# Optimization experiments

Hardware: AMD Instinct MI355X
Metric: run time of the kernel (lower is better)

The kernel has to match this reference:

```python
import jax, jax.numpy as jnp
import numpy as np

N_FFT = 512; HOP = 256; WIN = 512
FDRC = 0.5; ORDER = 5; SPKS = 2
NFREQ = N_FFT // 2 + 1           # 257
HID = 512
PROJ = 2 * ORDER * SPKS * NFREQ  # 5140
LN_EPS = 1e-5
_WINDOW = 0.5 - 0.5 * jnp.cos(2 * jnp.pi * jnp.arange(WIN) / WIN)  # periodic hann


def _stft(x):
    # x: [B, L] -> complex spec [B, F, T], center-padded (reflect), hann window
    pad = N_FFT // 2
    xp = jnp.pad(x, ((0, 0), (pad, pad)), mode='reflect')
    T = 1 + (xp.shape[1] - N_FFT) // HOP
    idx = jnp.arange(T)[:, None] * HOP + jnp.arange(N_FFT)[None, :]
    frames = xp[:, idx] * _WINDOW            # [B, T, n_fft]
    spec = jnp.fft.rfft(frames, axis=-1)     # [B, T, F]
    return spec.transpose(0, 2, 1)           # [B, F, T]


def _istft(spec, length):
    # spec: [B, F, T] complex -> waveform [B, length] via overlap-add with window-square norm
    pad = N_FFT // 2
    frames = jnp.fft.irfft(spec.transpose(0, 2, 1), n=N_FFT, axis=-1) * _WINDOW  # [B,T,n_fft]
    B, T, _ = frames.shape
    total = length + 2 * pad
    idx = (jnp.arange(T)[:, None] * HOP + jnp.arange(N_FFT)[None, :]).ravel()
    out = jnp.zeros((B, total), frames.dtype).at[:, idx].add(frames.reshape(B, -1))
    wsq = jnp.zeros((total,), frames.dtype).at[idx].add(jnp.tile(_WINDOW ** 2, T))
    seg = wsq[pad:pad + length]
    return out[:, pad:pad + length] / jnp.where(seg > 1e-11, seg, 1.0)


def _lstm(xs, W_ih, W_hh, b_ih, b_hh):
    # xs: [T, B, in]; torch gate order i,f,g,o; returns hidden sequence [T, B, H]
    T, B, _ = xs.shape
    H = W_hh.shape[1]
    xs_proj = xs @ W_ih.T + (b_ih + b_hh)    # hoist input projection out of scan

    def step(carry, xp_t):
        h, c = carry
        gates = xp_t + h @ W_hh.T
        i, f, g, o = jnp.split(gates, 4, axis=-1)
        c = jax.nn.sigmoid(f) * c + jax.nn.sigmoid(i) * jnp.tanh(g)
        h = jax.nn.sigmoid(o) * jnp.tanh(c)
        return (h, c), h

    init = (jnp.zeros((B, H), xs.dtype), jnp.zeros((B, H), xs.dtype))
    _, hs = jax.lax.scan(step, init, xs_proj)
    return hs


def setup_inputs() -> dict:
    key = jax.random.key(0)
    ks = jax.random.split(key, 14)
    s = 0.04  # ~ 1/sqrt(hidden)
    return {
        'x': jax.random.normal(ks[0], (32, 160000), dtype=jnp.float32),
        'ln_g': jnp.ones((NFREQ,), jnp.float32),
        'ln_b': jnp.zeros((NFREQ,), jnp.float32),
        'W_ih0': jax.random.normal(ks[1], (4 * HID, NFREQ), jnp.float32) * s,
        'W_hh0': jax.random.normal(ks[2], (4 * HID, HID), jnp.float32) * s,
        'b_ih0': jax.random.normal(ks[3], (4 * HID,), jnp.float32) * s,
        'b_hh0': jax.random.normal(ks[4], (4 * HID,), jnp.float32) * s,
        'W_ih1': jax.random.normal(ks[5], (4 * HID, HID), jnp.float32) * s,
        'W_hh1': jax.random.normal(ks[6], (4 * HID, HID), jnp.float32) * s,
        'b_ih1': jax.random.normal(ks[7], (4 * HID,), jnp.float32) * s,
        'b_hh1': jax.random.normal(ks[8], (4 * HID,), jnp.float32) * s,
        'proj_W': jax.random.normal(ks[9], (PROJ, HID), jnp.float32) * s,
        'proj_b': jax.random.normal(ks[10], (PROJ,), jnp.float32) * s,
    }


def reference(x, ln_g, ln_b, W_ih0, W_hh0, b_ih0, b_hh0,
              W_ih1, W_hh1, b_ih1, b_hh1, proj_W, proj_b):
    B, L = x.shape
    spec = _stft(x)                      # [B, F, T] complex
    T = spec.shape[-1]
    mag = jnp.abs(spec) ** FDRC          # [B, F, T]

    # full-band sequence model (pre-LN -> 2-layer LSTM -> proj -> tanh)
    h = mag.transpose(2, 0, 1)           # [T, B, F]
    mu = h.mean(-1, keepdims=True)
    var = h.var(-1, keepdims=True)
    h = (h - mu) / jnp.sqrt(var + LN_EPS) * ln_g + ln_b
    h = _lstm(h, W_ih0, W_hh0, b_ih0, b_hh0)
    h = _lstm(h, W_ih1, W_hh1, b_ih1, b_hh1)
    h = jnp.tanh(h @ proj_W.T + proj_b)  # [T, B, 2*d*s*F]
    fb = h.transpose(1, 2, 0)            # [B, 2*d*s*F, T]

    # deep-filter coefficients: 'b (c d s f) t -> b d s f t c' -> complex [B,d,s,F,T]
    coef = fb.reshape(B, 2, ORDER, SPKS, NFREQ, T)
    coef_c = jax.lax.complex(coef[:, 0], coef[:, 1])

    # unfold spectrogram along time with left pad of (order-1): [B, F, T, d]
    padded = jnp.pad(spec, ((0, 0), (0, 0), (ORDER - 1, 0)))
    spec_unf = jnp.stack([padded[:, :, d:d + T] for d in range(ORDER)], axis=-1)

    # out[b,s,f,t] = sum_d spec_unf[b,f,t,d] * coef[b,d,s,f,t]
    enh = jnp.einsum('bftd,bdsft->bsft', spec_unf, coef_c)  # [B, S, F, T]

    enh_y = _istft(enh.reshape(B * SPKS, NFREQ, T), L).reshape(B, SPKS, L)
    return enh_y
```

## Files before the change

### kernel.cpp

```cpp
#include <hip/hip_runtime.h>
#include <hip/hip_cooperative_groups.h>
#include <math.h>

#define BATCH 32
#define LEN   160000
#define NFFT  512
#define NT    626
#define NF    257
#define NFP   288
#define HID   512
#define PROJN 5140
#define TC    32
#define NCHUNK 20
#define K0    800
#define K1    1024
#define NLSTM 64
#define NWORK 192
#define NBLKT 256

typedef unsigned short ushort;
typedef __attribute__((ext_vector_type(8))) short short8;
typedef __attribute__((ext_vector_type(4))) float f32x4;

__device__ __forceinline__ float sigm(float x){ return 1.0f/(1.0f+expf(-x)); }
__device__ __forceinline__ ushort f2bf(float f){
  union{float f;unsigned u;} v; v.f=f;
  unsigned r = v.u + 0x7fffu + ((v.u>>16)&1u);
  return (ushort)(r>>16);
}

__global__ __launch_bounds__(256) void k_setup(float* tw, int* zr, int nz,
                                               float* h1slot0, int nh1s,
                                               float* outz, int nout,
                                               const float* __restrict__ Wih0, const float* __restrict__ Whh0,
                                               const float* __restrict__ bih0, const float* __restrict__ bhh0,
                                               const float* __restrict__ Wih1, const float* __restrict__ Whh1,
                                               const float* __restrict__ bih1, const float* __restrict__ bhh1,
                                               const float* __restrict__ projW,
                                               ushort* __restrict__ W0, ushort* __restrict__ W1,
                                               float* __restrict__ b0c, float* __restrict__ b1c,
                                               ushort* __restrict__ projWb){
  const int gsz = gridDim.x*256;
  int gid = blockIdx.x*256 + threadIdx.x;
  if (gid < 512){
    float ang = 6.28318530717958647692f * (float)gid / 512.0f;
    tw[gid]     = cosf(ang);
    tw[512+gid] = sinf(ang);
  }
  for (int j = gid; j < nz; j += gsz) zr[j] = 0;
  for (int j = gid; j < nh1s; j += gsz) h1slot0[j] = 0.f;
  for (int j = gid; j < nout; j += gsz) outz[j] = 0.f;
  const int n0 = 2048*K0, n1 = 2048*K1, n2 = PROJN*HID;
  for (int i = gid; i < n0 + n1 + 4096 + n2; i += gsz){
    if (i < n0){
      int r = i / K0, c = i - r*K0;
      float v = (c < 257) ? Wih0[(size_t)r*257 + c] : (c < NFP ? 0.f : Whh0[(size_t)r*512 + (c-NFP)]);
      W0[i] = f2bf(v);
    } else if (i < n0 + n1){
      int j = i - n0;
      int r = j / K1, c = j - r*K1;
      float v = (c < 512) ? Wih1[(size_t)r*512 + c] : Whh1[(size_t)r*512 + (c-512)];
      W1[j] = f2bf(v);
    } else if (i < n0 + n1 + 4096){
      int j = i - n0 - n1;
      if (j < 2048) b0c[j] = bih0[j] + bhh0[j];
      else          b1c[j-2048] = bih1[j-2048] + bhh1[j-2048];
    } else {
      int j = i - n0 - n1 - 4096;
      projWb[j] = f2bf(projW[j]);
    }
  }
}

__global__ __launch_bounds__(256) void k_stftln(const float* __restrict__ x, const float* __restrict__ tw,
                                                const float* __restrict__ g, const float* __restrict__ be,
                                                ushort* __restrict__ hlnb){
  int b = blockIdx.x / NT;
  int t = blockIdx.x % NT;
  __shared__ float fr[NFFT], mg[NF];
  __shared__ float red[16];
  const float* xb = x + (size_t)b*LEN;
  for (int n = threadIdx.x; n < NFFT; n += 256){
    int j = t*256 + n - 256;
    if (j < 0) j = -j;
    else if (j >= LEN) j = 2*LEN - 2 - j;
    fr[n] = xb[j] * (0.5f - 0.5f*tw[n]);
  }
  __syncthreads();
  float v=0.f, v2=0.f;
  for (int f = threadIdx.x; f < NF; f += 256){
    float c4 = tw[(4*f)&511], s4 = tw[512+((4*f)&511)];
    float cr0=1.f,            si0=0.f;
    float cr1=tw[f&511],      si1=tw[512+(f&511)];
    float cr2=tw[(2*f)&511],  si2=tw[512+((2*f)&511)];
    float cr3=tw[(3*f)&511],  si3=tw[512+((3*f)&511)];
    float ar0=0.f,ai0=0.f,ar1=0.f,ai1=0.f,ar2=0.f,ai2=0.f,ar3=0.f,ai3=0.f;
    #pragma unroll 4
    for (int n = 0; n < NFFT; n += 4){
      ar0 += fr[n  ]*cr0; ai0 -= fr[n  ]*si0;
      ar1 += fr[n+1]*cr1; ai1 -= fr[n+1]*si1;
      ar2 += fr[n+2]*cr2; ai2 -= fr[n+2]*si2;
      ar3 += fr[n+3]*cr3; ai3 -= fr[n+3]*si3;
      float tc, ts;
      tc = cr0*c4 - si0*s4; ts = cr0*s4 + si0*c4; cr0=tc; si0=ts;
      tc = cr1*c4 - si1*s4; ts = cr1*s4 + si1*c4; cr1=tc; si1=ts;
      tc = cr2*c4 - si2*s4; ts = cr2*s4 + si2*c4; cr2=tc; si2=ts;
      tc = cr3*c4 - si3*s4; ts = cr3*s4 + si3*c4; cr3=tc; si3=ts;
    }
    float ar = (ar0+ar1)+(ar2+ar3);
    float ai = (ai0+ai1)+(ai2+ai3);
    float m = sqrtf(sqrtf(ar*ar + ai*ai));
    mg[f]=m; v+=m; v2+=m*m;
  }
  for (int off=32; off; off>>=1){ v += __shfl_down(v,off); v2 += __shfl_down(v2,off); }
  int w = threadIdx.x >> 6;
  if ((threadIdx.x & 63)==0){ red[w]=v; red[8+w]=v2; }
  __syncthreads();
  if (threadIdx.x==0){
    float s  = red[0]+red[1]+red[2]+red[3];
    float s2 = red[8]+red[9]+red[10]+red[11];
    float mu = s/(float)NF;
    red[4]=mu;
    red[5]=rsqrtf(s2/(float)NF - mu*mu + 1e-5f);
  }
  __syncthreads();
  float mu=red[4], rs=red[5];
  size_t ob = ((size_t)t*BATCH + b)*NFP;
  for (int f=threadIdx.x; f<NFP; f+=256){
    float val = 0.f;
    if (f < NF) val = (mg[f]-mu)*rs*g[f] + be[f];
    hlnb[ob+f] = f2bf(val);
  }
}

__device__ void dev_stft_frame(const float* __restrict__ x, const float* __restrict__ tw,
                               float* __restrict__ spR, float* __restrict__ spI,
                               int tb0, int tt, int b, float* fr){
  int t = tb0 + tt;
  int tid = threadIdx.x;
  if (t < 0 || t >= NT){
    for (int f = tid; f < NF; f += 256){
      size_t o = ((size_t)b*NF + f)*36 + tt;
      spR[o]=0.f; spI[o]=0.f;
    }
    return;
  }
  const float* xb = x + (size_t)b*LEN;
  for (int n = tid; n < NFFT; n += 256){
    int j = t*256 + n - 256;
    if (j < 0) j = -j;
    else if (j >= LEN) j = 2*LEN - 2 - j;
    fr[n] = xb[j] * (0.5f - 0.5f*tw[n]);
  }
  __syncthreads();
  for (int f = tid; f < NF; f += 256){
    float c4 = tw[(4*f)&511], s4 = tw[512+((4*f)&511)];
    float cr0=1.f,            si0=0.f;
    float cr1=tw[f&511],      si1=tw[512+(f&511)];
    float cr2=tw[(2*f)&511],  si2=tw[512+((2*f)&511)];
    float cr3=tw[(3*f)&511],  si3=tw[512+((3*f)&511)];
    float ar0=0.f,ai0=0.f,ar1=0.f,ai1=0.f,ar2=0.f,ai2=0.f,ar3=0.f,ai3=0.f;
    #pragma unroll 4
    for (int n = 0; n < NFFT; n += 4){
      ar0 += fr[n  ]*cr0; ai0 -= fr[n  ]*si0;
      ar1 += fr[n+1]*cr1; ai1 -= fr[n+1]*si1;
      ar2 += fr[n+2]*cr2; ai2 -= fr[n+2]*si2;
      ar3 += fr[n+3]*cr3; ai3 -= fr[n+3]*si3;
      float tc, ts;
      tc = cr0*c4 - si0*s4; ts = cr0*s4 + si0*c4; cr0=tc; si0=ts;
      tc = cr1*c4 - si1*s4; ts = cr1*s4 + si1*c4; cr1=tc; si1=ts;
      tc = cr2*c4 - si2*s4; ts = cr2*s4 + si2*c4; cr2=tc; si2=ts;
      tc = cr3*c4 - si3*s4; ts = cr3*s4 + si3*c4; cr3=tc; si3=ts;
    }
    size_t o = ((size_t)b*NF + f)*36 + tt;
    spR[o] = (ar0+ar1)+(ar2+ar3);
    spI[o] = (ai0+ai1)+(ai2+ai3);
  }
  __syncthreads();
}

__device__ void dev_gemm_tile(const ushort* __restrict__ A, const ushort* __restrict__ Bb,
                              const float* __restrict__ bias, float* __restrict__ C,
                              int M, int N, int bx, int by){
  int bm = by*64, bn = bx*64;
  int wave = threadIdx.x >> 6, lane = threadIdx.x & 63;
  int wm = wave >> 1, wn = wave & 1;
  int col = lane & 15, kg = lane >> 4;
  f32x4 acc00={0.f,0.f,0.f,0.f}, acc01=acc00, acc10=acc00, acc11=acc00;
  const ushort* Ap = A + (size_t)(bm + wm*32)*512;
  int nr0 = bn + wn*32 + col;
  int nr1 = nr0 + 16;
  const ushort* Bp0 = Bb + (size_t)((nr0<N)?nr0:0)*512;
  const ushort* Bp1 = Bb + (size_t)((nr1<N)?nr1:0)*512;
  #pragma unroll 4
  for (int k0=0; k0<512; k0+=32){
    short8 a0 = *(const short8*)(Ap + (size_t)col*512 + k0 + kg*8);
    short8 a1 = *(const short8*)(Ap + (size_t)(16+col)*512 + k0 + kg*8);
    short8 b0 = *(const short8*)(Bp0 + k0 + kg*8);
    short8 b1 = *(const short8*)(Bp1 + k0 + kg*8);
    acc00 = __builtin_amdgcn_mfma_f32_16x16x32_bf16(a0, b0, acc00, 0, 0, 0);
    acc01 = __builtin_amdgcn_mfma_f32_16x16x32_bf16(a0, b1, acc01, 0, 0, 0);
    acc10 = __builtin_amdgcn_mfma_f32_16x16x32_bf16(a1, b0, acc10, 0, 0, 0);
    acc11 = __builtin_amdgcn_mfma_f32_16x16x32_bf16(a1, b1, acc11, 0, 0, 0);
  }
  #define STORE_ACC(ACC, MI, NI) { \
    int n = bn + wn*32 + (NI)*16 + col; \
    if (n < N){ \
      float bv = bias[n]; \
      _Pragma("unroll") \
      for (int j=0;j<4;j++){ \
        int m = bm + wm*32 + (MI)*16 + kg*4 + j; \
        C[(size_t)m*N + n] = tanhf(ACC[j] + bv); \
      } \
    } }
  STORE_ACC(acc00, 0, 0)
  STORE_ACC(acc01, 0, 1)
  STORE_ACC(acc10, 1, 0)
  STORE_ACC(acc11, 1, 1)
  #undef STORE_ACC
}

__device__ void dev_ifused_task(const float* __restrict__ prch,
    const float* __restrict__ spR, const float* __restrict__ spI,
    const float* __restrict__ tw, float* __restrict__ out, int tb0, int task,
    float* reb, float* imb){
  int tl = task >> 6;
  int b  = (task >> 1) & 31;
  int s  = task & 1;
  int tau = tb0 + 4 + tl;
  int tid = threadIdx.x;
  const float* p = prch + ((size_t)tl*BATCH + b)*PROJN;
  for (int f=tid; f<NF; f+=256){
    float ar=0.f, ai=0.f;
    size_t so = ((size_t)b*NF + f)*36;
    #pragma unroll
    for (int d=0; d<5; d++){
      int ts = tb0 + tl + d;
      if (ts >= 0){
        float sr=spR[so + tl + d], si=spI[so + tl + d];
        float cr=p[d*514 + s*257 + f];
        float ci=p[2570 + d*514 + s*257 + f];
        ar += sr*cr - si*ci;
        ai += sr*ci + si*cr;
      }
    }
    reb[f]=ar; imb[f]=ai;
  }
  __syncthreads();
  float* ob = out + (size_t)(b*2+s)*LEN;
  for (int n=tid; n<NFFT; n+=256){
    float c4 = tw[(4*n)&511], s4 = tw[512+((4*n)&511)];
    float crA=tw[n&511],     siA=tw[512+(n&511)];
    float crB=tw[(2*n)&511], siB=tw[512+((2*n)&511)];
    float crC=tw[(3*n)&511], siC=tw[512+((3*n)&511)];
    float crD=c4,            siD=s4;
    float a0=0.f,a1=0.f,a2=0.f,a3=0.f;
    #pragma unroll 4
    for (int m=0; m<63; m++){
      int k = 4*m+1;
      a0 += reb[k  ]*crA - imb[k  ]*siA;
      a1 += reb[k+1]*crB - imb[k+1]*siB;
      a2 += reb[k+2]*crC - imb[k+2]*siC;
      a3 += reb[k+3]*crD - imb[k+3]*siD;
      float tc, ts;
      tc = crA*c4 - siA*s4; ts = crA*s4 + siA*c4; crA=tc; siA=ts;
      tc = crB*c4 - siB*s4; ts = crB*s4 + siB*c4; crB=tc; siB=ts;
      tc = crC*c4 - siC*s4; ts = crC*s4 + siC*c4; crC=tc; siC=ts;
      tc = crD*c4 - siD*s4; ts = crD*s4 + siD*c4; crD=tc; siD=ts;
    }
    a0 += reb[253]*crA - imb[253]*siA;
    a1 += reb[254]*crB - imb[254]*siB;
    a2 += reb[255]*crC - imb[255]*siC;
    float acc = reb[0] + ((n&1) ? -reb[256] : reb[256]) + 2.f*((a0+a1)+(a2+a3));
    int pos = tau*256 - 256 + n;
    if (pos >= 0 && pos < LEN)
      atomicAdd(ob + pos, acc * (1.0f/512.0f) * (0.5f - 0.5f*tw[n&511]));
  }
  __syncthreads();
}

__global__ __launch_bounds__(256, 1) void k_mega(const ushort* __restrict__ hlnb,
    const ushort* __restrict__ W0g, const ushort* __restrict__ W1g,
    const float* __restrict__ b0c, const float* __restrict__ b1c,
    ushort* __restrict__ h0b, ushort* __restrict__ h1b, ushort* __restrict__ h1hist,
    unsigned* __restrict__ flagsA, unsigned* __restrict__ epoch, unsigned* __restrict__ done,
    const float* __restrict__ x, const float* __restrict__ tw,
    const ushort* __restrict__ projWb, const float* __restrict__ projb,
    float* __restrict__ spR, float* __restrict__ spI, float* __restrict__ prch,
    float* __restrict__ out){
  __shared__ ushort Wlds0[32*808];
  __shared__ ushort Wlds1[32*1032];
  __shared__ float pc0[32][33];
  __shared__ float pc1[32][33];
  __shared__ float fr[NFFT];
  __shared__ float reb[NF], imb[NF];

  const int tid  = threadIdx.x;
  const int bid  = blockIdx.x;

  if (bid < NLSTM){
    const int u0   = bid << 3;
    const int wave = tid >> 6;
    const int lane = tid & 63;
    const int col  = lane & 15;
    const int kg   = lane >> 4;
    const int mh   = wave & 1;
    const int nh   = wave >> 1;
    const int arow = (mh<<4) + col;
    const int nlo  = (nh<<4) + col;

    for (int v = tid; v < 3200; v += 256){
      int r = v/100, c8 = v - r*100;
      int grow = ((r>>3)<<9) + u0 + (r&7);
      *(short8*)&Wlds0[r*808 + c8*8] = *(const short8*)(W0g + (size_t)grow*K0 + c8*8);
    }
    for (int v = tid; v < 4096; v += 256){
      int r = v>>7, c8 = v&127;
      int grow = ((r>>3)<<9) + u0 + (r&7);
      *(short8*)&Wlds1[r*1032 + c8*8] = *(const short8*)(W1g + (size_t)grow*K1 + c8*8);
    }
    const int bb = tid & 31;
    const int ul = tid >> 5;
    const int u  = u0 + ul;
    float bc0r[4], bc1r[4];
    #pragma unroll
    for (int g=0; g<4; g++){ bc0r[g] = b0c[(g<<9)+u]; bc1r[g] = b1c[(g<<9)+u]; }
    float c0r = 0.f, c1r = 0.f;
    const ushort* wb0 = &Wlds0[nlo*808];
    const ushort* wb1 = &Wlds1[nlo*1032];
    __syncthreads();

    f32x4 acc0x = {0.f,0.f,0.f,0.f};
    {
      const ushort* xt = hlnb;
      #pragma unroll
      for (int kt=0; kt<9; kt++){
        short8 a = *(const short8*)(xt + arow*NFP + kt*32 + kg*8);
        short8 b = *(const short8*)(wb0 + kt*32 + kg*8);
        acc0x = __builtin_amdgcn_mfma_f32_16x16x32_bf16(a, b, acc0x, 0, 0, 0);
      }
    }

    for (int t = 0; t <= NT; ++t){
      const ushort* h0p = h0b + (size_t)((t-1)&1)*(BATCH*HID);
      f32x4 acc0 = acc0x;
      f32x4 acc1 = {0.f,0.f,0.f,0.f};
      if (t >= 1){
        const ushort* h1p = h1b + (size_t)((t-2)&1)*(BATCH*HID);
        #pragma unroll
        for (int kt=0; kt<16; kt++){
          short8 a = *(const short8*)(h0p + arow*HID + kt*32 + kg*8);
          short8 b = *(const short8*)(wb1 + kt*32 + kg*8);
          acc1 = __builtin_amdgcn_mfma_f32_16x16x32_bf16(a, b, acc1, 0, 0, 0);
        }
        #pragma unroll
        for (int kt=0; kt<16; kt++){
          short8 a = *(const short8*)(h1p + arow*HID + kt*32 + kg*8);
          short8 b = *(const short8*)(wb1 + 512 + kt*32 + kg*8);
          acc1 = __builtin_amdgcn_mfma_f32_16x16x32_bf16(a, b, acc1, 0, 0, 0);
        }
      }
      if (t < NT){
        #pragma unroll
        for (int kt=0; kt<16; kt++){
          short8 a = *(const short8*)(h0p + arow*HID + kt*32 + kg*8);
          short8 b = *(const short8*)(wb0 + 288 + kt*32 + kg*8);
          acc0 = __builtin_amdgcn_mfma_f32_16x16x32_bf16(a, b, acc0, 0, 0, 0);
        }
      }
      if (t < NT){
        #pragma unroll
        for (int j=0;j<4;j++) pc0[(mh<<4)+(kg<<2)+j][nlo] = acc0[j];
      }
      if (t >= 1){
        #pragma unroll
        for (int j=0;j<4;j++) pc1[(mh<<4)+(kg<<2)+j][nlo] = acc1[j];
      }
      __syncthreads();
      if (t < NT){
        float p0 = pc0[bb][0*8+ul] + bc0r[0];
        float p1 = pc0[bb][1*8+ul] + bc0r[1];
        float p2 = pc0[bb][2*8+ul] + bc0r[2];
        float p3 = pc0[bb][3*8+ul] + bc0r[3];
        float cn = sigm(p1)*c0r + sigm(p0)*tanhf(p2);
        float hn = sigm(p3)*tanhf(cn);
        c0r = cn;
        h0b[(size_t)(t&1)*(BATCH*HID) + bb*HID + u] = f2bf(hn);
      }
      if (t >= 1){
        float p0 = pc1[bb][0*8+ul] + bc1r[0];
        float p1 = pc1[bb][1*8+ul] + bc1r[1];
        float p2 = pc1[bb][2*8+ul] + bc1r[2];
        float p3 = pc1[bb][3*8+ul] + bc1r[3];
        float cn = sigm(p1)*c1r + sigm(p0)*tanhf(p2);
        float hn = sigm(p3)*tanhf(cn);
        c1r = cn;
        ushort hb = f2bf(hn);
        h1b[(size_t)((t-1)&1)*(BATCH*HID) + bb*HID + u] = hb;
        __builtin_nontemporal_store(hb, h1hist + (size_t)t*(BATCH*HID) + bb*HID + u);
      }
      __syncthreads();
      if (tid == 0)
        __hip_atomic_store(&flagsA[bid*32], (unsigned)(t+1), __ATOMIC_RELEASE, __HIP_MEMORY_SCOPE_AGENT);
      acc0x = f32x4{0.f,0.f,0.f,0.f};
      if (t+1 < NT){
        const ushort* xt = hlnb + (size_t)(t+1)*BATCH*NFP;
        #pragma unroll
        for (int kt=0; kt<9; kt++){
          short8 a = *(const short8*)(xt + arow*NFP + kt*32 + kg*8);
          short8 b = *(const short8*)(wb0 + kt*32 + kg*8);
          acc0x = __builtin_amdgcn_mfma_f32_16x16x32_bf16(a, b, acc0x, 0, 0, 0);
        }
      }
      if (wave == 0){
        unsigned tgt = (unsigned)(t+1);
        while (true){
          unsigned v = __hip_atomic_load(&flagsA[lane*32], __ATOMIC_RELAXED, __HIP_MEMORY_SCOPE_AGENT);
          if (__all(v >= tgt)) break;
          __builtin_amdgcn_s_sleep(1);
        }
        if (bid == 0 && lane == 0)
          __hip_atomic_store(epoch, (unsigned)(t+1), __ATOMIC_RELAXED, __HIP_MEMORY_SCOPE_AGENT);
        (void)__hip_atomic_load(&flagsA[lane*32], __ATOMIC_ACQUIRE, __HIP_MEMORY_SCOPE_AGENT);
      }
      asm volatile("" ::: "memory");
      __syncthreads();
    }
    return;
  }

  const int w = bid - NLSTM;
  for (int c = 0; c < NCHUNK; ++c){
    int tcc = (c == NCHUNK-1) ? (NT - c*TC) : TC;
    int tb0 = c*TC - 4;
    unsigned need = (unsigned)(c*TC + tcc + 1);
    if (tid == 0){
      while (__hip_atomic_load(epoch, __ATOMIC_RELAXED, __HIP_MEMORY_SCOPE_AGENT) < need)
        __builtin_amdgcn_s_sleep(32);
      (void)__hip_atomic_load(epoch, __ATOMIC_ACQUIRE, __HIP_MEMORY_SCOPE_AGENT);
    }
    __syncthreads();
    for (int i = w; i < 36*BATCH; i += NWORK)
      dev_stft_frame(x, tw, spR, spI, tb0, i % 36, i / 36, fr);
    {
      unsigned* d0 = done + (c*3+0)*32;
      __syncthreads();
      if (tid == 0){
        __hip_atomic_fetch_add(d0, 1u, __ATOMIC_RELEASE, __HIP_MEMORY_SCOPE_AGENT);
        while (__hip_atomic_load(d0, __ATOMIC_RELAXED, __HIP_MEMORY_SCOPE_AGENT) < NWORK)
          __builtin_amdgcn_s_sleep(4);
        (void)__hip_atomic_load(d0, __ATOMIC_ACQUIRE, __HIP_MEMORY_SCOPE_AGENT);
      }
      __syncthreads();
    }
    {
      int gy = (tcc*BATCH)/64;
      int ntask = 81*gy;
      const ushort* A = h1hist + ((size_t)(c*TC)+1)*BATCH*HID;
      for (int i = w; i < ntask; i += NWORK)
        dev_gemm_tile(A, projWb, projb, prch, tcc*BATCH, PROJN, i % 81, i / 81);
      unsigned* d1 = done + (c*3+1)*32;
      __syncthreads();
      if (tid == 0){
        __hip_atomic_fetch_add(d1, 1u, __ATOMIC_RELEASE, __HIP_MEMORY_SCOPE_AGENT);
        while (__hip_atomic_load(d1, __ATOMIC_RELAXED, __HIP_MEMORY_SCOPE_AGENT) < NWORK)
          __builtin_amdgcn_s_sleep(4);
        (void)__hip_atomic_load(d1, __ATOMIC_ACQUIRE, __HIP_MEMORY_SCOPE_AGENT);
      }
      __syncthreads();
    }
    {
      for (int i = w; i < tcc*64; i += NWORK)
        dev_ifused_task(prch, spR, spI, tw, out, tb0, i, reb, imb);
      unsigned* d2 = done + (c*3+2)*32;
      __syncthreads();
      if (tid == 0){
        __hip_atomic_fetch_add(d2, 1u, __ATOMIC_RELEASE, __HIP_MEMORY_SCOPE_AGENT);
        while (__hip_atomic_load(d2, __ATOMIC_RELAXED, __HIP_MEMORY_SCOPE_AGENT) < NWORK)
          __builtin_amdgcn_s_sleep(4);
        (void)__hip_atomic_load(d2, __ATOMIC_ACQUIRE, __HIP_MEMORY_SCOPE_AGENT);
      }
      __syncthreads();
    }
  }
  for (size_t i = (size_t)w*256 + tid; i < (size_t)64*LEN; i += (size_t)NWORK*256){
    int m = (int)(i % LEN) & 255;
    float cm = tw[m];
    float w1 = 0.5f - 0.5f*cm;
    float w2 = 0.5f + 0.5f*cm;
    out[i] = out[i] / (w1*w1 + w2*w2);
  }
}

extern "C" void kernel_launch(void* const* d_in, const int* in_sizes, int n_in,
                              void* d_out, int out_size, void* d_ws, size_t ws_size,
                              hipStream_t stream){
  const float* x     = (const float*)d_in[0];
  const float* ln_g  = (const float*)d_in[1];
  const float* ln_b  = (const float*)d_in[2];
  const float* Wih0  = (const float*)d_in[3];
  const float* Whh0  = (const float*)d_in[4];
  const float* bih0  = (const float*)d_in[5];
  const float* bhh0  = (const float*)d_in[6];
  const float* Wih1  = (const float*)d_in[7];
  const float* Whh1  = (const float*)d_in[8];
  const float* bih1  = (const float*)d_in[9];
  const float* bhh1  = (const float*)d_in[10];
  const float* projW = (const float*)d_in[11];
  const float* projb = (const float*)d_in[12];

  char* base = (char*)d_ws;
  size_t off = 0;
  auto carve = [&](size_t bytes)->char*{
    char* p = base + off;
    off += (bytes + 255) & ~(size_t)255;
    return p;
  };
  float*  tw     = (float*) carve(1024*4);
  ushort* hlnb   = (ushort*)carve((size_t)NT*BATCH*NFP*2);
  ushort* W0     = (ushort*)carve((size_t)2048*K0*2);
  ushort* W1     = (ushort*)carve((size_t)2048*K1*2);
  float*  b0c    = (float*) carve(2048*4);
  float*  b1c    = (float*) carve(2048*4);
  ushort* projWb = (ushort*)carve((size_t)PROJN*HID*2);
  size_t zoff0 = off;
  ushort* h0b    = (ushort*)carve((size_t)2*BATCH*HID*2);
  ushort* h1b    = (ushort*)carve((size_t)2*BATCH*HID*2);
  unsigned* flagsA = (unsigned*)carve(NLSTM*32*4);
  unsigned* epoch  = (unsigned*)carve(128);
  unsigned* done   = (unsigned*)carve(NCHUNK*3*32*4);
  size_t zlen = off - zoff0;
  ushort* h1hist = (ushort*)carve((size_t)(NT+1)*BATCH*HID*2);
  float*  spR    = (float*) carve((size_t)BATCH*NF*36*4);
  float*  spI    = (float*) carve((size_t)BATCH*NF*36*4);
  float*  prch   = (float*) carve((size_t)TC*BATCH*PROJN*4);

  k_setup<<<4096, 256, 0, stream>>>(tw, (int*)(base + zoff0), (int)(zlen/4),
                                    (float*)h1hist, BATCH*HID/2,
                                    (float*)d_out, out_size,
                                    Wih0, Whh0, bih0, bhh0, Wih1, Whh1, bih1, bhh1,
                                    projW, W0, W1, b0c, b1c, projWb);
  k_stftln<<<BATCH*NT, 256, 0, stream>>>(x, tw, ln_g, ln_b, hlnb);

  {
    float* outp = (float*)d_out;
    void* args[] = { (void*)&hlnb, (void*)&W0, (void*)&W1, (void*)&b0c, (void*)&b1c,
                     (void*)&h0b, (void*)&h1b, (void*)&h1hist,
                     (void*)&flagsA, (void*)&epoch, (void*)&done,
                     (void*)&x, (void*)&tw, (void*)&projWb, (void*)&projb,
                     (void*)&spR, (void*)&spI, (void*)&prch, (void*)&outp };
    hipLaunchCooperativeKernel(reinterpret_cast<void*>(k_mega), dim3(NBLKT), dim3(256),
                               args, 0, stream);
  }
}
```

Before: 9.261 ms.

## Split LSTM layers onto separate block groups with decoupled flag synchronisation

Instead of each of 64 blocks computing both LSTM layers in lockstep, 32 blocks now own layer 0 and 32 own layer 1, each with 16 hidden units per block. Layer 0 runs ahead, tracked by its own flag array, with a 4-deep h0 ring buffer and bounded lag against layer 1's flags. The aim is to shorten each block's per-step critical path (one layer's GEMV instead of two) and let the layers pipeline. The trade-offs are a larger per-block LDS footprint via one unified shared buffer, and two sets of grid-wide flag polling.

```diff
diff --git a/kernel.cpp b/kernel.cpp
--- a/kernel.cpp
+++ b/kernel.cpp
@@ -14,6 +14,8 @@
 #define NCHUNK 20
 #define K0    800
 #define K1    1024
+#define NL0   32
+#define NL1   32
 #define NLSTM 64
 #define NWORK 192
 #define NBLKT 256
@@ -283,152 +285,215 @@
     const ushort* __restrict__ W0g, const ushort* __restrict__ W1g,
     const float* __restrict__ b0c, const float* __restrict__ b1c,
     ushort* __restrict__ h0b, ushort* __restrict__ h1b, ushort* __restrict__ h1hist,
-    unsigned* __restrict__ flagsA, unsigned* __restrict__ epoch, unsigned* __restrict__ done,
+    unsigned* __restrict__ flagsA, unsigned* __restrict__ flagsB,
+    unsigned* __restrict__ epoch, unsigned* __restrict__ done,
     const float* __restrict__ x, const float* __restrict__ tw,
     const ushort* __restrict__ projWb, const float* __restrict__ projb,
     float* __restrict__ spR, float* __restrict__ spI, float* __restrict__ prch,
     float* __restrict__ out){
-  __shared__ ushort Wlds0[32*808];
-  __shared__ ushort Wlds1[32*1032];
-  __shared__ float pc0[32][33];
-  __shared__ float pc1[32][33];
-  __shared__ float fr[NFFT];
-  __shared__ float reb[NF], imb[NF];
+  __shared__ __align__(16) char smem[141312];
 
   const int tid  = threadIdx.x;
   const int bid  = blockIdx.x;
 
-  if (bid < NLSTM){
-    const int u0   = bid << 3;
-    const int wave = tid >> 6;
-    const int lane = tid & 63;
-    const int col  = lane & 15;
-    const int kg   = lane >> 4;
-    const int mh   = wave & 1;
-    const int nh   = wave >> 1;
-    const int arow = (mh<<4) + col;
-    const int nlo  = (nh<<4) + col;
-
-    for (int v = tid; v < 3200; v += 256){
-      int r = v/100, c8 = v - r*100;
-      int grow = ((r>>3)<<9) + u0 + (r&7);
-      *(short8*)&Wlds0[r*808 + c8*8] = *(const short8*)(W0g + (size_t)grow*K0 + c8*8);
-    }
-    for (int v = tid; v < 4096; v += 256){
-      int r = v>>7, c8 = v&127;
-      int grow = ((r>>3)<<9) + u0 + (r&7);
-      *(short8*)&Wlds1[r*1032 + c8*8] = *(const short8*)(W1g + (size_t)grow*K1 + c8*8);
-    }
+  if (bid < NL0 + NL1){
+    const int layer = (bid < NL0) ? 0 : 1;
+    const int lb    = layer ? (bid - NL0) : bid;
+    const int u0    = lb << 4;
+    const int wave  = tid >> 6;
+    const int lane  = tid & 63;
+    const int col   = lane & 15;
+    const int kg    = lane >> 4;
+    ushort* Wl = (ushort*)smem;
+    float (*pc)[68] = (float(*)[68])(smem + 132352);
+
+    const int K = layer ? K1 : K0;
+    const int WPAD = layer ? 1032 : 808;
+    const ushort* Wg = layer ? W1g : W0g;
+    {
+      int nv8 = 64 * (K >> 3);
+      int kv8 = K >> 3;
+      for (int v = tid; v < nv8; v += 256){
+        int r = v / kv8, c8 = v - r*kv8;
+        int grow = ((r>>4)<<9) + u0 + (r&15);
+        *(short8*)&Wl[r*WPAD + c8*8] = *(const short8*)(Wg + (size_t)grow*K + c8*8);
+      }
+    }
+    const ushort* wb = &Wl[(size_t)(wave*16 + col)*WPAD];
     const int bb = tid & 31;
-    const int ul = tid >> 5;
-    const int u  = u0 + ul;
-    float bc0r[4], bc1r[4];
+    const int ua = tid >> 5;
+    const float* bc = layer ? b1c : b0c;
+    float bcA[4], bcB[4];
     #pragma unroll
-    for (int g=0; g<4; g++){ bc0r[g] = b0c[(g<<9)+u]; bc1r[g] = b1c[(g<<9)+u]; }
-    float c0r = 0.f, c1r = 0.f;
-    const ushort* wb0 = &Wlds0[nlo*808];
-    const ushort* wb1 = &Wlds1[nlo*1032];
+    for (int g=0; g<4; g++){
+      bcA[g] = bc[(g<<9) + u0 + ua];
+      bcB[g] = bc[(g<<9) + u0 + 8 + ua];
+    }
+    float cA = 0.f, cB = 0.f;
     __syncthreads();
 
-    f32x4 acc0x = {0.f,0.f,0.f,0.f};
-    {
-      const ushort* xt = hlnb;
-      #pragma unroll
-      for (int kt=0; kt<9; kt++){
-        short8 a = *(const short8*)(xt + arow*NFP + kt*32 + kg*8);
-        short8 b = *(const short8*)(wb0 + kt*32 + kg*8);
-        acc0x = __builtin_amdgcn_mfma_f32_16x16x32_bf16(a, b, acc0x, 0, 0, 0);
-      }
-    }
-
-    for (int t = 0; t <= NT; ++t){
-      const ushort* h0p = h0b + (size_t)((t-1)&1)*(BATCH*HID);
-      f32x4 acc0 = acc0x;
-      f32x4 acc1 = {0.f,0.f,0.f,0.f};
-      if (t >= 1){
-        const ushort* h1p = h1b + (size_t)((t-2)&1)*(BATCH*HID);
+    if (layer == 0){
+      f32x4 ax0 = {0.f,0.f,0.f,0.f}, ax1 = ax0;
+      {
+        const ushort* xt = hlnb;
+        #pragma unroll
+        for (int kt=0; kt<9; kt++){
+          short8 b = *(const short8*)(wb + kt*32 + kg*8);
+          short8 a0 = *(const short8*)(xt + (size_t)col*NFP + kt*32 + kg*8);
+          short8 a1 = *(const short8*)(xt + (size_t)(16+col)*NFP + kt*32 + kg*8);
+          ax0 = __builtin_amdgcn_mfma_f32_16x16x32_bf16(a0, b, ax0, 0, 0, 0);
+          ax1 = __builtin_amdgcn_mfma_f32_16x16x32_bf16(a1, b, ax1, 0, 0, 0);
+        }
+      }
+      for (int t = 0; t < NT; ++t){
+        const ushort* h0p = h0b + (size_t)((t-1)&3)*(BATCH*HID);
+        f32x4 acc0 = ax0, acc1 = ax1;
         #pragma unroll
         for (int kt=0; kt<16; kt++){
-          short8 a = *(const short8*)(h0p + arow*HID + kt*32 + kg*8);
-          short8 b = *(const short8*)(wb1 + kt*32 + kg*8);
-          acc1 = __builtin_amdgcn_mfma_f32_16x16x32_bf16(a, b, acc1, 0, 0, 0);
-        }
+          short8 b = *(const short8*)(wb + 288 + kt*32 + kg*8);
+          short8 a0 = *(const short8*)(h0p + (size_t)col*HID + kt*32 + kg*8);
+          short8 a1 = *(const short8*)(h0p + (size_t)(16+col)*HID + kt*32 + kg*8);
+          acc0 = __builtin_amdgcn_mfma_f32_16x16x32_bf16(a0, b, acc0, 0, 0, 0);
+          acc1 = __builtin_amdgcn_mfma_f32_16x16x32_bf16(a1, b, acc1, 0, 0, 0);
+        }
+        #pragma unroll
+        for (int j=0;j<4;j++){
+          pc[(kg<<2)+j][wave*16+col]      = acc0[j];
+          pc[16+(kg<<2)+j][wave*16+col]   = acc1[j];
+        }
+        __syncthreads();
+        {
+          float p0 = pc[bb][0*16+ua] + bcA[0];
+          float p1 = pc[bb][1*16+ua] + bcA[1];
+          float p2 = pc[bb][2*16+ua] + bcA[2];
+          float p3 = pc[bb][3*16+ua] + bcA[3];
+          float cn = sigm(p1)*cA + sigm(p0)*tanhf(p2);
+          float hn = sigm(p3)*tanhf(cn);
+          cA = cn;
+          h0b[(size_t)(t&3)*(BATCH*HID) + bb*HID + u0 + ua] = f2bf(hn);
+          p0 = pc[bb][0*16+8+ua] + bcB[0];
+          p1 = pc[bb][1*16+8+ua] + bcB[1];
+          p2 = pc[bb][2*16+8+ua] + bcB[2];
+          p3 = pc[bb][3*16+8+ua] + bcB[3];
+          cn = sigm(p1)*cB + sigm(p0)*tanhf(p2);
+          hn = sigm(p3)*tanhf(cn);
+          cB = cn;
+          h0b[(size_t)(t&3)*(BATCH*HID) + bb*HID + u0 + 8 + ua] = f2bf(hn);
+        }
+        __syncthreads();
+        if (tid == 0)
+          __hip_atomic_store(&flagsA[lb*32], (unsigned)(t+1), __ATOMIC_RELEASE, __HIP_MEMORY_SCOPE_AGENT);
+        ax0 = f32x4{0.f,0.f,0.f,0.f}; ax1 = ax0;
+        if (t+1 < NT){
+          const ushort* xt = hlnb + (size_t)(t+1)*BATCH*NFP;
+          #pragma unroll
+          for (int kt=0; kt<9; kt++){
+            short8 b = *(const short8*)(wb + kt*32 + kg*8);
+            short8 a0 = *(const short8*)(xt + (size_t)col*NFP + kt*32 + kg*8);
+            short8 a1 = *(const short8*)(xt + (size_t)(16+col)*NFP + kt*32 + kg*8);
+            ax0 = __builtin_amdgcn_mfma_f32_16x16x32_bf16(a0, b, ax0, 0, 0, 0);
+            ax1 = __builtin_amdgcn_mfma_f32_16x16x32_bf16(a1, b, ax1, 0, 0, 0);
+          }
+        }
+        if (wave == 0){
+          unsigned tgtA = (unsigned)(t+1);
+          unsigned tgtB = (t >= 2) ? (unsigned)(t-2) : 0u;
+          while (true){
+            unsigned vA = (lane < 32) ? __hip_atomic_load(&flagsA[lane*32], __ATOMIC_RELAXED, __HIP_MEMORY_SCOPE_AGENT) : 0xFFFFFFFFu;
+            unsigned vB = (lane < 32) ? __hip_atomic_load(&flagsB[lane*32], __ATOMIC_RELAXED, __HIP_MEMORY_SCOPE_AGENT) : 0xFFFFFFFFu;
+            if (__all(vA >= tgtA) && __all(vB >= tgtB)) break;
+            __builtin_amdgcn_s_sleep(1);
+          }
+          (void)__hip_atomic_load(&flagsA[(lane&31)*32], __ATOMIC_ACQUIRE, __HIP_MEMORY_SCOPE_AGENT);
+        }
+        asm volatile("" ::: "memory");
+        __syncthreads();
+      }
+      return;
+    } else {
+      for (int tau = 0; tau < NT; ++tau){
+        if (wave == 0){
+          unsigned tgt = (unsigned)(tau+1);
+          while (true){
+            unsigned v = (lane < 32) ? __hip_atomic_load(&flagsA[lane*32], __ATOMIC_RELAXED, __HIP_MEMORY_SCOPE_AGENT) : 0xFFFFFFFFu;
+            if (__all(v >= tgt)) break;
+            __builtin_amdgcn_s_sleep(1);
+          }
+          (void)__hip_atomic_load(&flagsA[(lane&31)*32], __ATOMIC_ACQUIRE, __HIP_MEMORY_SCOPE_AGENT);
+        }
+        asm volatile("" ::: "memory");
+        __syncthreads();
+        const ushort* h0p = h0b + (size_t)(tau&3)*(BATCH*HID);
+        const ushort* h1p = h1b + (size_t)((tau-1)&1)*(BATCH*HID);
+        f32x4 acc0 = {0.f,0.f,0.f,0.f}, acc1 = acc0;
         #pragma unroll
         for (int kt=0; kt<16; kt++){
-          short8 a = *(const short8*)(h1p + arow*HID + kt*32 + kg*8);
-          short8 b = *(const short8*)(wb1 + 512 + kt*32 + kg*8);
-          acc1 = __builtin_amdgcn_mfma_f32_16x16x32_bf16(a, b, acc1, 0, 0, 0);
-        }
-      }
-      if (t < NT){
+          short8 b = *(const short8*)(wb + kt*32 + kg*8);
+          short8 a0 = *(const short8*)(h0p + (size_t)col*HID + kt*32 + kg*8);
+          short8 a1 = *(const short8*)(h0p + (size_t)(16+col)*HID + kt*32 + kg*8);
+          acc0 = __builtin_amdgcn_mfma_f32_16x16x32_bf16(a0, b, acc0, 0, 0, 0);
+          acc1 = __builtin_amdgcn_mfma_f32_16x16x32_bf16(a1, b, acc1, 0, 0, 0);
+        }
         #pragma unroll
         for (int kt=0; kt<16; kt++){
-          short8 a = *(const short8*)(h0p + arow*HID + kt*32 + kg*8);
-          short8 b = *(const short8*)(wb0 + 288 + kt*32 + kg*8);
-          acc0 = __builtin_amdgcn_mfma_f32_16x16x32_bf16(a, b, acc0, 0, 0, 0);
-        }
-      }
-      if (t < NT){
+          short8 b = *(const short8*)(wb + 512 + kt*32 + kg*8);
+          short8 a0 = *(const short8*)(h1p + (size_t)col*HID + kt*32 + kg*8);
+          short8 a1 = *(const short8*)(h1p + (size_t)(16+col)*HID + kt*32 + kg*8);
+          acc0 = __builtin_amdgcn_mfma_f32_16x16x32_bf16(a0, b, acc0, 0, 0, 0);
+          acc1 = __builtin_amdgcn_mfma_f32_16x16x32_bf16(a1, b, acc1, 0, 0, 0);
+        }
         #pragma unroll
-        for (int j=0;j<4;j++) pc0[(mh<<4)+(kg<<2)+j][nlo] = acc0[j];
-      }
-      if (t >= 1){
-        #pragma unroll
-        for (int j=0;j<4;j++) pc1[(mh<<4)+(kg<<2)+j][nlo] = acc1[j];
-      }
-      __syncthreads();
-      if (t < NT){
-        float p0 = pc0[bb][0*8+ul] + bc0r[0];
-        float p1 = pc0[bb][1*8+ul] + bc0r[1];
-        float p2 = pc0[bb][2*8+ul] + bc0r[2];
-        float p3 = pc0[bb][3*8+ul] + bc0r[3];
-        float cn = sigm(p1)*c0r + sigm(p0)*tanhf(p2);
-        float hn = sigm(p3)*tanhf(cn);
-        c0r = cn;
-        h0b[(size_t)(t&1)*(BATCH*HID) + bb*HID + u] = f2bf(hn);
-      }
-      if (t >= 1){
-        float p0 = pc1[bb][0*8+ul] + bc1r[0];
-        float p1 = pc1[bb][1*8+ul] + bc1r[1];
-        float p2 = pc1[bb][2*8+ul] + bc1r[2];
-        float p3 = pc1[bb][3*8+ul] + bc1r[3];
-        float cn = sigm(p1)*c1r + sigm(p0)*tanhf(p2);
-        float hn = sigm(p3)*tanhf(cn);
-        c1r = cn;
-        ushort hb = f2bf(hn);
-        h1b[(size_t)((t-1)&1)*(BATCH*HID) + bb*HID + u] = hb;
-        __builtin_nontemporal_store(hb, h1hist + (size_t)t*(BATCH*HID) + bb*HID + u);
-      }
-      __syncthreads();
-      if (tid == 0)
-        __hip_atomic_store(&flagsA[bid*32], (unsigned)(t+1), __ATOMIC_RELEASE, __HIP_MEMORY_SCOPE_AGENT);
-      acc0x = f32x4{0.f,0.f,0.f,0.f};
-      if (t+1 < NT){
-        const ushort* xt = hlnb + (size_t)(t+1)*BATCH*NFP;
-        #pragma unroll
-        for (int kt=0; kt<9; kt++){
-          short8 a = *(const short8*)(xt + arow*NFP + kt*32 + kg*8);
-          short8 b = *(const short8*)(wb0 + kt*32 + kg*8);
-          acc0x = __builtin_amdgcn_mfma_f32_16x16x32_bf16(a, b, acc0x, 0, 0, 0);
-        }
-      }
-      if (wave == 0){
-        unsigned tgt = (unsigned)(t+1);
-        while (true){
-          unsigned v = __hip_atomic_load(&flagsA[lane*32], __ATOMIC_RELAXED, __HIP_MEMORY_SCOPE_AGENT);
-          if (__all(v >= tgt)) break;
-          __builtin_amdgcn_s_sleep(1);
-        }
-        if (bid == 0 && lane == 0)
-          __hip_atomic_store(epoch, (unsigned)(t+1), __ATOMIC_RELAXED, __HIP_MEMORY_SCOPE_AGENT);
-        (void)__hip_atomic_load(&flagsA[lane*32], __ATOMIC_ACQUIRE, __HIP_MEMORY_SCOPE_AGENT);
-      }
-      asm volatile("" ::: "memory");
-      __syncthreads();
-    }
-    return;
-  }
-
+        for (int j=0;j<4;j++){
+          pc[(kg<<2)+j][wave*16+col]      = acc0[j];
+          pc[16+(kg<<2)+j][wave*16+col]   = acc1[j];
+        }
+        __syncthreads();
+        {
+          float p0 = pc[bb][0*16+ua] + bcA[0];
+          float p1 = pc[bb][1*16+ua] + bcA[1];
+          float p2 = pc[bb][2*16+ua] + bcA[2];
+          float p3 = pc[bb][3*16+ua] + bcA[3];
+          float cn = sigm(p1)*cA + sigm(p0)*tanhf(p2);
+          float hn = sigm(p3)*tanhf(cn);
+          cA = cn;
+          ushort hb = f2bf(hn);
+          h1b[(size_t)(tau&1)*(BATCH*HID) + bb*HID + u0 + ua] = hb;
+          __builtin_nontemporal_store(hb, h1hist + (size_t)(tau+1)*(BATCH*HID) + bb*HID + u0 + ua);
+          p0 = pc[bb][0*16+8+ua] + bcB[0];
+          p1 = pc[bb][1*16+8+ua] + bcB[1];
+          p2 = pc[bb][2*16+8+ua] + bcB[2];
+          p3 = pc[bb][3*16+8+ua] + bcB[3];
+          cn = sigm(p1)*cB + sigm(p0)*tanhf(p2);
+          hn = sigm(p3)*tanhf(cn);
+          cB = cn;
+          hb = f2bf(hn);
+          h1b[(size_t)(tau&1)*(BATCH*HID) + bb*HID + u0 + 8 + ua] = hb;
+          __builtin_nontemporal_store(hb, h1hist + (size_t)(tau+1)*(BATCH*HID) + bb*HID + u0 + 8 + ua);
+        }
+        __syncthreads();
+        if (tid == 0)
+          __hip_atomic_store(&flagsB[lb*32], (unsigned)(tau+1), __ATOMIC_RELEASE, __HIP_MEMORY_SCOPE_AGENT);
+        if (wave == 0){
+          unsigned tgt = (unsigned)(tau+1);
+          while (true){
+            unsigned v = (lane < 32) ? __hip_atomic_load(&flagsB[lane*32], __ATOMIC_RELAXED, __HIP_MEMORY_SCOPE_AGENT) : 0xFFFFFFFFu;
+            if (__all(v >= tgt)) break;
+            __builtin_amdgcn_s_sleep(1);
+          }
+          if (lb == 0 && lane == 0)
+            __hip_atomic_store(epoch, (unsigned)(tau+2), __ATOMIC_RELAXED, __HIP_MEMORY_SCOPE_AGENT);
+          (void)__hip_atomic_load(&flagsB[(lane&31)*32], __ATOMIC_ACQUIRE, __HIP_MEMORY_SCOPE_AGENT);
+        }
+        asm volatile("" ::: "memory");
+        __syncthreads();
+      }
+      return;
+    }
+  }
+
+  float* fr  = (float*)smem;
+  float* reb = fr + 512;
+  float* imb = reb + 260;
   const int w = bid - NLSTM;
   for (int c = 0; c < NCHUNK; ++c){
     int tcc = (c == NCHUNK-1) ? (NT - c*TC) : TC;
@@ -524,9 +589,10 @@
   float*  b1c    = (float*) carve(2048*4);
   ushort* projWb = (ushort*)carve((size_t)PROJN*HID*2);
   size_t zoff0 = off;
-  ushort* h0b    = (ushort*)carve((size_t)2*BATCH*HID*2);
+  ushort* h0b    = (ushort*)carve((size_t)4*BATCH*HID*2);
   ushort* h1b    = (ushort*)carve((size_t)2*BATCH*HID*2);
-  unsigned* flagsA = (unsigned*)carve(NLSTM*32*4);
+  unsigned* flagsA = (unsigned*)carve(NL0*32*4);
+  unsigned* flagsB = (unsigned*)carve(NL1*32*4);
   unsigned* epoch  = (unsigned*)carve(128);
   unsigned* done   = (unsigned*)carve(NCHUNK*3*32*4);
   size_t zlen = off - zoff0;
@@ -546,7 +612,7 @@
     float* outp = (float*)d_out;
     void* args[] = { (void*)&hlnb, (void*)&W0, (void*)&W1, (void*)&b0c, (void*)&b1c,
                      (void*)&h0b, (void*)&h1b, (void*)&h1hist,
-                     (void*)&flagsA, (void*)&epoch, (void*)&done,
+                     (void*)&flagsA, (void*)&flagsB, (void*)&epoch, (void*)&done,
                      (void*)&x, (void*)&tw, (void*)&projWb, (void*)&projb,
                      (void*)&spR, (void*)&spI, (void*)&prch, (void*)&outp };
     hipLaunchCooperativeKernel(reinterpret_cast<void*>(k_mega), dim3(NBLKT), dim3(256),
```

After: 9.949 ms. 7.4% more time.
